# Kernel optimization log

Measured on AMD Instinct MI355X. Metric: run time of the kernel, lower is better.

Reference implementation:

```python
import jax, jax.numpy as jnp
from jax import lax
import numpy as np

SEQ, B, IN, H = 512, 64, 1024, 1024


def setup_inputs() -> dict:
    key = jax.random.key(0)
    ks = jax.random.split(key, 9)
    s = 0.02
    return {
        "x":   jax.random.normal(ks[0], (SEQ, B, IN), dtype=jnp.float32),
        # layer 0: Linear(input_dim, hidden) and Linear(hidden, hidden)
        "Wi0": jax.random.normal(ks[1], (H, IN), dtype=jnp.float32) * s,
        "bi0": jax.random.normal(ks[2], (H,), dtype=jnp.float32) * s,
        "Wh0": jax.random.normal(ks[3], (H, H), dtype=jnp.float32) * s,
        "bh0": jax.random.normal(ks[4], (H,), dtype=jnp.float32) * s,
        # layer 1: Linear(hidden, hidden) twice
        "Wi1": jax.random.normal(ks[5], (H, H), dtype=jnp.float32) * s,
        "bi1": jax.random.normal(ks[6], (H,), dtype=jnp.float32) * s,
        "Wh1": jax.random.normal(ks[7], (H, H), dtype=jnp.float32) * s,
        "bh1": jax.random.normal(ks[8], (H,), dtype=jnp.float32) * s,
    }


def reference(x, Wi0, bi0, Wh0, bh0, Wi1, bi1, Wh1, bh1):
    # x: [seq, batch, in]; two-layer tanh RNN, time-major, zero initial hidden.
    batch = x.shape[1]
    hdim = Wh0.shape[0]
    h0 = jnp.zeros((2, batch, hdim), dtype=x.dtype)

    def step(h_prev, x_t):
        h1 = jnp.tanh(x_t @ Wi0.T + bi0 + h_prev[0] @ Wh0.T + bh0)
        h2 = jnp.tanh(h1 @ Wi1.T + bi1 + h_prev[1] @ Wh1.T + bh1)
        return jnp.stack([h1, h2], axis=0), h2

    h_final, outputs = lax.scan(step, h0, x)
    return outputs, h_final
```

## Files before the change

kernel.cpp:

```cpp
#include <hip/hip_runtime.h>


#define SEQ 512
#define BATCH 64
#define HID 1024
#define BH (BATCH * HID)
#define DEPTH 8

typedef __attribute__((ext_vector_type(8))) short short8;
typedef __attribute__((ext_vector_type(4))) float f32x4;
typedef __attribute__((ext_vector_type(4))) unsigned int u32x4;

__device__ __forceinline__ unsigned short f32_to_bf16_rne(float f) {
    unsigned int u = __float_as_uint(f);
    u += 0x7FFFu + ((u >> 16) & 1u);
    return (unsigned short)(u >> 16);
}

__device__ __forceinline__ short8 cvt8(float4 f0, float4 f1) {
    short8 w;
    w[0] = (short)f32_to_bf16_rne(f0.x);
    w[1] = (short)f32_to_bf16_rne(f0.y);
    w[2] = (short)f32_to_bf16_rne(f0.z);
    w[3] = (short)f32_to_bf16_rne(f0.w);
    w[4] = (short)f32_to_bf16_rne(f1.x);
    w[5] = (short)f32_to_bf16_rne(f1.y);
    w[6] = (short)f32_to_bf16_rne(f1.z);
    w[7] = (short)f32_to_bf16_rne(f1.w);
    return w;
}

__device__ __forceinline__ void ld_cc16(short8& d, const unsigned short* p) {
    asm volatile("global_load_dwordx4 %0, %1, off sc0 sc1"
                 : "=v"(d) : "v"(p) : "memory");
}

__device__ __forceinline__ void vm_wait0() {
    asm volatile("s_waitcnt vmcnt(0)" ::: "memory");
    __builtin_amdgcn_sched_barrier(0);
}

__device__ __forceinline__ void st_cc16(unsigned short* p, unsigned v) {
    asm volatile("global_store_short %0, %1, off sc0 sc1"
                 :: "v"(p), "v"(v) : "memory");
}

__device__ __forceinline__ unsigned min_u16x4(u32x4 w, unsigned mn) {
    #pragma unroll
    for (int j = 0; j < 4; ++j) {
        unsigned lo = w[j] & 0xFFFFu, hi = w[j] >> 16;
        mn = mn < lo ? mn : lo;
        mn = mn < hi ? mn : hi;
    }
    return mn;
}

__device__ __forceinline__ void wait_one32(const unsigned short* f, int target) {
    if (target <= 0) return;
    for (;;) {
        u32x4 r[4];
        #pragma unroll
        for (int i = 0; i < 4; ++i)
            asm volatile("global_load_dwordx4 %0, %1, off sc0 sc1"
                         : "=v"(r[i]) : "v"((const unsigned int*)f + i * 4) : "memory");
        asm volatile("s_waitcnt vmcnt(0)" ::: "memory");
        __builtin_amdgcn_sched_barrier(0);
        unsigned mn = 0xFFFFu;
        #pragma unroll
        for (int i = 0; i < 4; ++i) mn = min_u16x4(r[i], mn);
        if ((int)mn >= target) return;
        __builtin_amdgcn_s_sleep(1);
    }
}

__device__ __forceinline__ void wait_two32(const unsigned short* f0, int t0,
                                           const unsigned short* f1, int t1) {
    if (t0 <= 0 && t1 <= 0) return;
    for (;;) {
        u32x4 r0[4], r1[4];
        #pragma unroll
        for (int i = 0; i < 4; ++i)
            asm volatile("global_load_dwordx4 %0, %1, off sc0 sc1"
                         : "=v"(r0[i]) : "v"((const unsigned int*)f0 + i * 4) : "memory");
        #pragma unroll
        for (int i = 0; i < 4; ++i)
            asm volatile("global_load_dwordx4 %0, %1, off sc0 sc1"
                         : "=v"(r1[i]) : "v"((const unsigned int*)f1 + i * 4) : "memory");
        asm volatile("s_waitcnt vmcnt(0)" ::: "memory");
        __builtin_amdgcn_sched_barrier(0);
        unsigned m0 = 0xFFFFu, m1 = 0xFFFFu;
        #pragma unroll
        for (int i = 0; i < 4; ++i) { m0 = min_u16x4(r0[i], m0); m1 = min_u16x4(r1[i], m1); }
        if ((int)m0 >= t0 && (int)m1 >= t1) return;
        __builtin_amdgcn_s_sleep(1);
    }
}

#define MFMA16(W, A, ACC) \
    ACC = __builtin_amdgcn_mfma_f32_16x16x32_bf16((W), (A), (ACC), 0, 0, 0)

__device__ __forceinline__ void ring_mm16(const unsigned short* pr, size_t aoff,
                                          const short8* wreg, f32x4& acc) {
    short8 a[16];
    #pragma unroll
    for (int k = 0; k < 16; ++k)
        ld_cc16(a[k], pr + aoff + k * 32);
    vm_wait0();
    #pragma unroll
    for (int k = 0; k < 16; ++k)
        MFMA16(wreg[k], a[k], acc);
}

__global__ void cvt_f32_bf16(const float* __restrict__ src,
                             unsigned short* __restrict__ dst, int n4) {
    int i = blockIdx.x * blockDim.x + threadIdx.x;
    int stride = gridDim.x * blockDim.x;
    for (; i < n4; i += stride) {
        float4 f = ((const float4*)src)[i];
        ushort4 o;
        o.x = f32_to_bf16_rne(f.x);
        o.y = f32_to_bf16_rne(f.y);
        o.z = f32_to_bf16_rne(f.z);
        o.w = f32_to_bf16_rne(f.w);
        ((ushort4*)dst)[i] = o;
    }
}

__global__ void init_ws(uint4* __restrict__ p, int n16) {
    int i = blockIdx.x * blockDim.x + threadIdx.x;
    if (i < n16) p[i] = make_uint4(0u, 0u, 0u, 0u);
}

__global__ __launch_bounds__(512, 1) void rnn_mfma(
    const float* __restrict__ x,
    const unsigned short* __restrict__ xb, int use_xb,
    const float* __restrict__ Wi0, const float* __restrict__ bi0,
    const float* __restrict__ Wh0, const float* __restrict__ bh0,
    const float* __restrict__ Wi1, const float* __restrict__ bi1,
    const float* __restrict__ Wh1, const float* __restrict__ bh1,
    float* __restrict__ out,
    unsigned short* __restrict__ rings,
    unsigned short* __restrict__ flags)
{
    unsigned short* h1ring = rings;
    unsigned short* h2ring = rings + DEPTH * BH;

    const int tid   = threadIdx.x;
    const int wg    = blockIdx.x;
    const int layer = wg >> 7;
    const int rg4   = (wg >> 5) & 3;
    const int nb32  = wg & 31;
    const int wv    = tid >> 6;
    const int lane  = tid & 63;
    const int fb    = wv >> 2;
    const int srcw  = (wv >> 1) & 1;
    const int kh    = wv & 1;

    unsigned short* gL0 = flags + (0 * 4 + rg4) * 64;
    unsigned short* gL1 = flags + (1 * 4 + rg4) * 64;
    unsigned short* ep_self = (layer ? gL1 : gL0) + nb32;

    const float* Wsel = layer ? (srcw ? Wh1 : Wi1) : (srcw ? Wh0 : Wi0);
    const int f_w = nb32 * 32 + fb * 16 + (lane & 15);
    const int kcb = kh * 512 + (lane >> 4) * 8;
    short8 wreg[16];
    {
        const float* rw = Wsel + (size_t)f_w * HID + kcb;
        #pragma unroll
        for (int ks = 0; ks < 16; ++ks)
            wreg[ks] = cvt8(*(const float4*)(rw + ks * 32),
                            *(const float4*)(rw + ks * 32 + 4));
    }

    const int arow = rg4 * 16 + (lane & 15);
    const size_t aoff = (size_t)arow * HID + kcb;

    const int r_feat = tid & 31;
    const int r_row  = tid >> 5;
    const int gf     = nb32 * 32 + r_feat;
    const int grow   = rg4 * 16 + r_row;
    const float* biv = layer ? bi1 : bi0;
    const float* bhv = layer ? bh1 : bh0;
    const float biasv = biv[gf] + bhv[gf];
    const int rw_base = (r_feat >> 4) * 4;

    __shared__ float red[8][16][17];

    for (int s = 0; s < SEQ; ++s) {
        f32x4 acc = {0.f, 0.f, 0.f, 0.f};

        if (layer == 0 && srcw == 0) {
            if (use_xb) {
                const unsigned short* px = xb + (size_t)s * BH + aoff;
                #pragma unroll
                for (int ks = 0; ks < 16; ++ks) {
                    short8 a = *(const short8*)(px + ks * 32);
                    MFMA16(wreg[ks], a, acc);
                }
            } else {
                const float* px = x + (size_t)s * BH + aoff;
                #pragma unroll
                for (int ks = 0; ks < 16; ++ks) {
                    short8 a = cvt8(*(const float4*)(px + ks * 32),
                                    *(const float4*)(px + ks * 32 + 4));
                    MFMA16(wreg[ks], a, acc);
                }
            }
        } else if (layer == 0) {
            if (lane == 0) wait_two32(gL0, s, gL1, s - (DEPTH - 1));
            ring_mm16(h1ring + (size_t)((s - 1) & (DEPTH - 1)) * BH, aoff, wreg, acc);
        } else if (srcw == 1) {
            if (lane == 0) wait_one32(gL1, s);
            ring_mm16(h2ring + (size_t)((s - 1) & (DEPTH - 1)) * BH, aoff, wreg, acc);
        } else {
            if (lane == 0) wait_one32(gL0, s + 1);
            ring_mm16(h1ring + (size_t)(s & (DEPTH - 1)) * BH, aoff, wreg, acc);
        }

        #pragma unroll
        for (int r = 0; r < 4; ++r)
            red[wv][4 * (lane >> 4) + r][lane & 15] = acc[r];
        __syncthreads();

        float v;
        {
            const int ff = r_feat & 15;
            v = red[rw_base][ff][r_row] + red[rw_base + 1][ff][r_row]
              + red[rw_base + 2][ff][r_row] + red[rw_base + 3][ff][r_row] + biasv;
            v = tanhf(v);
            unsigned short* ring_self =
                (layer ? h2ring : h1ring) + (size_t)(s & (DEPTH - 1)) * BH;
            st_cc16(ring_self + (size_t)grow * HID + gf, f32_to_bf16_rne(v));
        }

        asm volatile("s_waitcnt vmcnt(0)" ::: "memory");
        __builtin_amdgcn_sched_barrier(0);
        __syncthreads();
        if (tid == 0)
            st_cc16(ep_self, (unsigned)(s + 1));

        if (layer == 1) {
            out[(size_t)s * BH + (size_t)grow * HID + gf] = v;
            if (s == SEQ - 1)
                out[(size_t)SEQ * BH + BH + (size_t)grow * HID + gf] = v;
        } else if (s == SEQ - 1) {
            out[(size_t)SEQ * BH + (size_t)grow * HID + gf] = v;
        }
    }
}

extern "C" void kernel_launch(void* const* d_in, const int* in_sizes, int n_in,
                              void* d_out, int out_size, void* d_ws, size_t ws_size,
                              hipStream_t stream) {
    const float* xp   = (const float*)d_in[0];
    const float* Wi0p = (const float*)d_in[1];
    const float* bi0p = (const float*)d_in[2];
    const float* Wh0p = (const float*)d_in[3];
    const float* bh0p = (const float*)d_in[4];
    const float* Wi1p = (const float*)d_in[5];
    const float* bi1p = (const float*)d_in[6];
    const float* Wh1p = (const float*)d_in[7];
    const float* bh1p = (const float*)d_in[8];
    float* outp = (float*)d_out;

    unsigned short* rings = (unsigned short*)d_ws;
    const size_t ring_bytes = (size_t)2 * DEPTH * BH * sizeof(unsigned short);
    unsigned short* flags = (unsigned short*)((char*)d_ws + ring_bytes);
    const size_t flag_pad = 4096;
    unsigned short* xb = (unsigned short*)((char*)d_ws + ring_bytes + flag_pad);
    const size_t xb_bytes = (size_t)SEQ * BH * 2;
    const int use_xb = (ws_size >= ring_bytes + flag_pad + xb_bytes) ? 1 : 0;

    {
        const int n16 = (int)((ring_bytes + flag_pad) / 16);
        init_ws<<<(n16 + 255) / 256, 256, 0, stream>>>((uint4*)d_ws, n16);
    }
    if (use_xb)
        cvt_f32_bf16<<<2048, 256, 0, stream>>>(xp, xb, SEQ * BH / 4);

    rnn_mfma<<<dim3(256), dim3(512), 0, stream>>>(
        xp, xb, use_xb,
        Wi0p, bi0p, Wh0p, bh0p, Wi1p, bi1p, Wh1p, bh1p,
        outp, rings, flags);
}
```

Before: 3.853 ms.

## Tag ring entries with step counters so consumers validate data inline

Each ring element becomes a 32-bit word that packs the bf16 hidden value with a 16-bit step tag. Consumers spin on the loaded data until every tag matches, then repack the bf16 halves for the MFMA. This drops the producer's vmcnt(0) wait before the flag store and lets correctness rest on the per-element tags rather than only on flag ordering. The cost is twice the ring traffic, possible repeated loads of 16 dwordx4 per chunk while spinning, and ring depth cut from 8 to 4 to fit the larger entries.

```diff
diff --git a/kernel.cpp b/kernel.cpp
--- a/kernel.cpp
+++ b/kernel.cpp
@@ -5,7 +5,7 @@
 #define BATCH 64
 #define HID 1024
 #define BH (BATCH * HID)
-#define DEPTH 8
+#define DEPTH 4
 
 typedef __attribute__((ext_vector_type(8))) short short8;
 typedef __attribute__((ext_vector_type(4))) float f32x4;
@@ -30,16 +30,15 @@
     return w;
 }
 
-__device__ __forceinline__ void ld_cc16(short8& d, const unsigned short* p) {
-    asm volatile("global_load_dwordx4 %0, %1, off sc0 sc1"
-                 : "=v"(d) : "v"(p) : "memory");
-}
-
 __device__ __forceinline__ void vm_wait0() {
     asm volatile("s_waitcnt vmcnt(0)" ::: "memory");
     __builtin_amdgcn_sched_barrier(0);
 }
 
+__device__ __forceinline__ void st_cc32(unsigned* p, unsigned v) {
+    asm volatile("global_store_dword %0, %1, off sc0 sc1"
+                 :: "v"(p), "v"(v) : "memory");
+}
 __device__ __forceinline__ void st_cc16(unsigned short* p, unsigned v) {
     asm volatile("global_store_short %0, %1, off sc0 sc1"
                  :: "v"(p), "v"(v) : "memory");
@@ -99,16 +98,42 @@
 #define MFMA16(W, A, ACC) \
     ACC = __builtin_amdgcn_mfma_f32_16x16x32_bf16((W), (A), (ACC), 0, 0, 0)
 
-__device__ __forceinline__ void ring_mm16(const unsigned short* pr, size_t aoff,
-                                          const short8* wreg, f32x4& acc) {
-    short8 a[16];
+__device__ __forceinline__ void ring_mm_tag(const unsigned* base, unsigned tag,
+                                            const short8* wreg, f32x4& acc) {
     #pragma unroll
-    for (int k = 0; k < 16; ++k)
-        ld_cc16(a[k], pr + aoff + k * 32);
-    vm_wait0();
-    #pragma unroll
-    for (int k = 0; k < 16; ++k)
-        MFMA16(wreg[k], a[k], acc);
+    for (int c = 0; c < 2; ++c) {
+        u32x4 lo[8], hi[8];
+        for (;;) {
+            #pragma unroll
+            for (int k = 0; k < 8; ++k) {
+                const unsigned* p = base + (c * 8 + k) * 32;
+                asm volatile("global_load_dwordx4 %0, %1, off sc0 sc1"
+                             : "=v"(lo[k]) : "v"(p) : "memory");
+                asm volatile("global_load_dwordx4 %0, %1, off sc0 sc1"
+                             : "=v"(hi[k]) : "v"(p + 4) : "memory");
+            }
+            asm volatile("s_waitcnt vmcnt(0)" ::: "memory");
+            __builtin_amdgcn_sched_barrier(0);
+            unsigned d = 0;
+            #pragma unroll
+            for (int k = 0; k < 8; ++k) {
+                #pragma unroll
+                for (int j = 0; j < 4; ++j) { d |= lo[k][j] ^ tag; d |= hi[k][j] ^ tag; }
+            }
+            if (__all((d & 0xFFFFu) == 0u)) break;
+            __builtin_amdgcn_s_sleep(1);
+        }
+        #pragma unroll
+        for (int k = 0; k < 8; ++k) {
+            u32x4 pk;
+            pk[0] = (lo[k][0] >> 16) | (lo[k][1] & 0xFFFF0000u);
+            pk[1] = (lo[k][2] >> 16) | (lo[k][3] & 0xFFFF0000u);
+            pk[2] = (hi[k][0] >> 16) | (hi[k][1] & 0xFFFF0000u);
+            pk[3] = (hi[k][2] >> 16) | (hi[k][3] & 0xFFFF0000u);
+            short8 a = __builtin_bit_cast(short8, pk);
+            MFMA16(wreg[c * 8 + k], a, acc);
+        }
+    }
 }
 
 __global__ void cvt_f32_bf16(const float* __restrict__ src,
@@ -139,11 +164,11 @@
     const float* __restrict__ Wi1, const float* __restrict__ bi1,
     const float* __restrict__ Wh1, const float* __restrict__ bh1,
     float* __restrict__ out,
-    unsigned short* __restrict__ rings,
+    unsigned* __restrict__ rings32,
     unsigned short* __restrict__ flags)
 {
-    unsigned short* h1ring = rings;
-    unsigned short* h2ring = rings + DEPTH * BH;
+    unsigned* h1r = rings32;
+    unsigned* h2r = rings32 + DEPTH * BH;
 
     const int tid   = threadIdx.x;
     const int wg    = blockIdx.x;
@@ -208,13 +233,16 @@
             }
         } else if (layer == 0) {
             if (lane == 0) wait_two32(gL0, s, gL1, s - (DEPTH - 1));
-            ring_mm16(h1ring + (size_t)((s - 1) & (DEPTH - 1)) * BH, aoff, wreg, acc);
+            ring_mm_tag(h1r + (size_t)((s - 1) & (DEPTH - 1)) * BH + aoff,
+                        (unsigned)s, wreg, acc);
         } else if (srcw == 1) {
             if (lane == 0) wait_one32(gL1, s);
-            ring_mm16(h2ring + (size_t)((s - 1) & (DEPTH - 1)) * BH, aoff, wreg, acc);
+            ring_mm_tag(h2r + (size_t)((s - 1) & (DEPTH - 1)) * BH + aoff,
+                        (unsigned)s, wreg, acc);
         } else {
             if (lane == 0) wait_one32(gL0, s + 1);
-            ring_mm16(h1ring + (size_t)(s & (DEPTH - 1)) * BH, aoff, wreg, acc);
+            ring_mm_tag(h1r + (size_t)(s & (DEPTH - 1)) * BH + aoff,
+                        (unsigned)(s + 1), wreg, acc);
         }
 
         #pragma unroll
@@ -228,13 +256,11 @@
             v = red[rw_base][ff][r_row] + red[rw_base + 1][ff][r_row]
               + red[rw_base + 2][ff][r_row] + red[rw_base + 3][ff][r_row] + biasv;
             v = tanhf(v);
-            unsigned short* ring_self =
-                (layer ? h2ring : h1ring) + (size_t)(s & (DEPTH - 1)) * BH;
-            st_cc16(ring_self + (size_t)grow * HID + gf, f32_to_bf16_rne(v));
-        }
-
-        asm volatile("s_waitcnt vmcnt(0)" ::: "memory");
-        __builtin_amdgcn_sched_barrier(0);
+            unsigned tagged = ((unsigned)f32_to_bf16_rne(v) << 16) | (unsigned)(s + 1);
+            unsigned* ring_self = (layer ? h2r : h1r) + (size_t)(s & (DEPTH - 1)) * BH;
+            st_cc32(ring_self + (size_t)grow * HID + gf, tagged);
+        }
+
         __syncthreads();
         if (tid == 0)
             st_cc16(ep_self, (unsigned)(s + 1));
@@ -263,8 +289,8 @@
     const float* bh1p = (const float*)d_in[8];
     float* outp = (float*)d_out;
 
-    unsigned short* rings = (unsigned short*)d_ws;
-    const size_t ring_bytes = (size_t)2 * DEPTH * BH * sizeof(unsigned short);
+    unsigned* rings32 = (unsigned*)d_ws;
+    const size_t ring_bytes = (size_t)2 * DEPTH * BH * sizeof(unsigned);
     unsigned short* flags = (unsigned short*)((char*)d_ws + ring_bytes);
     const size_t flag_pad = 4096;
     unsigned short* xb = (unsigned short*)((char*)d_ws + ring_bytes + flag_pad);
@@ -281,5 +307,5 @@
     rnn_mfma<<<dim3(256), dim3(512), 0, stream>>>(
         xp, xb, use_xb,
         Wi0p, bi0p, Wh0p, bh0p, Wi1p, bi1p, Wh1p, bh1p,
-        outp, rings, flags);
-}
+        outp, rings32, flags);
+}
```

New measurement: 8.180 ms. 2.12x slower.
